# Kernel tuning notes

Hardware: AMD Instinct MI355X
Metric: run time of the kernel (lower is better)

The kernel has to match this reference:

```python
import jax, jax.numpy as jnp
import numpy as np

GRID_H, GRID_W, NUM_FEATURES = 512, 512, 4
N_POINTS = 8388608


def setup_inputs() -> dict:
    key = jax.random.key(0)
    k1, k2 = jax.random.split(key)
    feature_grid = jax.random.normal(k1, (GRID_H, GRID_W, NUM_FEATURES), dtype=jnp.float32)
    # continuous sample locations in grid coordinates [0, dim-1)
    u = jax.random.uniform(k2, (N_POINTS, 2), dtype=jnp.float32)
    location = u * jnp.array([GRID_H - 1, GRID_W - 1], dtype=jnp.float32)
    return {"feature_grid": feature_grid, "location": location}


def bilinear_sample(feature_grid, location):
    H, W, F = feature_grid.shape
    x = location[:, 0]
    y = location[:, 1]
    x0 = jnp.clip(jnp.floor(x), 0, H - 2).astype(jnp.int32)
    y0 = jnp.clip(jnp.floor(y), 0, W - 2).astype(jnp.int32)
    x1 = x0 + 1
    y1 = y0 + 1
    fx = (x - x0.astype(x.dtype))[:, None]  # [N,1]
    fy = (y - y0.astype(y.dtype))[:, None]
    # gather 4 corners: each [N,F]
    f00 = feature_grid[x0, y0]
    f01 = feature_grid[x0, y1]
    f10 = feature_grid[x1, y0]
    f11 = feature_grid[x1, y1]
    return (f00 * (1 - fx) * (1 - fy)
            + f01 * (1 - fx) * fy
            + f10 * fx * (1 - fy)
            + f11 * fx * fy)


def reference(feature_grid, location):
    return bilinear_sample(feature_grid, location)
```

## Files before the change

kernel.cpp:

```cpp
#include <hip/hip_runtime.h>
#include <hip/hip_fp16.h>

#define GRID_H 512
#define GRID_W 512
#define NCELLS (GRID_H * GRID_W)

typedef float f32x4 __attribute__((ext_vector_type(4)));

__global__ __launch_bounds__(256) void convert_grid_kernel(
    const float4* __restrict__ g,
    uint2* __restrict__ gh,
    int ncells)
{
    int i = blockIdx.x * blockDim.x + threadIdx.x;
    if (i < ncells) {
        float4 v = g[i];
        __half2 lo = __floats2half2_rn(v.x, v.y);
        __half2 hi = __floats2half2_rn(v.z, v.w);
        uint2 o;
        o.x = *reinterpret_cast<const unsigned int*>(&lo);
        o.y = *reinterpret_cast<const unsigned int*>(&hi);
        gh[i] = o;
    }
}

struct alignas(8) RowPair { __half2 h[4]; };

__device__ __forceinline__ f32x4 sample_point(const char* __restrict__ gh, float x, float y)
{
    float fx0 = fminf(fmaxf(floorf(x), 0.0f), (float)(GRID_H - 2));
    float fy0 = fminf(fmaxf(floorf(y), 0.0f), (float)(GRID_W - 2));
    int x0 = (int)fx0;
    int y0 = (int)fy0;
    float fx = x - fx0;
    float fy = y - fy0;

    int c0 = x0 * GRID_W + y0;

    RowPair r0 = *reinterpret_cast<const RowPair*>(gh + (size_t)c0 * 8);
    RowPair r1 = *reinterpret_cast<const RowPair*>(gh + (size_t)(c0 + GRID_W) * 8);

    float2 a0 = __half22float2(r0.h[0]);
    float2 a1 = __half22float2(r0.h[1]);
    float2 b0 = __half22float2(r0.h[2]);
    float2 b1 = __half22float2(r0.h[3]);
    float2 c0f = __half22float2(r1.h[0]);
    float2 c1f = __half22float2(r1.h[1]);
    float2 d0 = __half22float2(r1.h[2]);
    float2 d1 = __half22float2(r1.h[3]);

    float gx = 1.0f - fx;
    float gy = 1.0f - fy;
    float w00 = gx * gy;
    float w01 = gx * fy;
    float w10 = fx * gy;
    float w11 = fx * fy;

    f32x4 r;
    r.x = a0.x * w00 + b0.x * w01 + c0f.x * w10 + d0.x * w11;
    r.y = a0.y * w00 + b0.y * w01 + c0f.y * w10 + d0.y * w11;
    r.z = a1.x * w00 + b1.x * w01 + c1f.x * w10 + d1.x * w11;
    r.w = a1.y * w00 + b1.y * w01 + c1f.y * w10 + d1.y * w11;
    return r;
}

__global__ __launch_bounds__(256) void bilinear_half_kernel(
    const char* __restrict__ gh,
    const f32x4* __restrict__ loc2,
    f32x4* __restrict__ out,
    int npair, int n)
{
    const int stride = gridDim.x * blockDim.x;
    for (int i = blockIdx.x * blockDim.x + threadIdx.x; i < npair; i += stride) {
        f32x4 p = __builtin_nontemporal_load(&loc2[i]);
        f32x4 rA = sample_point(gh, p.x, p.y);
        f32x4 rB = sample_point(gh, p.z, p.w);
        __builtin_nontemporal_store(rA, &out[2 * i]);
        __builtin_nontemporal_store(rB, &out[2 * i + 1]);
    }
    if ((n & 1) && blockIdx.x == 0 && threadIdx.x == 0) {
        const float2* locs = (const float2*)loc2;
        float2 p = locs[n - 1];
        f32x4 r = sample_point(gh, p.x, p.y);
        out[n - 1] = r;
    }
}

__global__ __launch_bounds__(256) void bilinear_f32_kernel(
    const float4* __restrict__ grid,
    const float2* __restrict__ loc,
    float4* __restrict__ out,
    int n)
{
    const int stride = gridDim.x * blockDim.x;
    for (int i = blockIdx.x * blockDim.x + threadIdx.x; i < n; i += stride) {
        float2 p = loc[i];
        float fx0 = fminf(fmaxf(floorf(p.x), 0.0f), (float)(GRID_H - 2));
        float fy0 = fminf(fmaxf(floorf(p.y), 0.0f), (float)(GRID_W - 2));
        int x0 = (int)fx0, y0 = (int)fy0;
        float fx = p.x - fx0, fy = p.y - fy0;
        int base = x0 * GRID_W + y0;
        float4 f00 = grid[base];
        float4 f01 = grid[base + 1];
        float4 f10 = grid[base + GRID_W];
        float4 f11 = grid[base + GRID_W + 1];
        float gx = 1.0f - fx, gy = 1.0f - fy;
        float w00 = gx * gy, w01 = gx * fy, w10 = fx * gy, w11 = fx * fy;
        float4 r;
        r.x = f00.x * w00 + f01.x * w01 + f10.x * w10 + f11.x * w11;
        r.y = f00.y * w00 + f01.y * w01 + f10.y * w10 + f11.y * w11;
        r.z = f00.z * w00 + f01.z * w01 + f10.z * w10 + f11.z * w11;
        r.w = f00.w * w00 + f01.w * w01 + f10.w * w10 + f11.w * w11;
        out[i] = r;
    }
}

extern "C" void kernel_launch(void* const* d_in, const int* in_sizes, int n_in,
                              void* d_out, int out_size, void* d_ws, size_t ws_size,
                              hipStream_t stream) {
    const float* grid_f32 = (const float*)d_in[0];
    const float* loc_f32  = (const float*)d_in[1];

    int n = in_sizes[1] / 2;
    const size_t gh_bytes = (size_t)NCELLS * 8;

    if (ws_size >= gh_bytes) {
        {
            int threads = 256;
            int blocks = (NCELLS + threads - 1) / threads;
            convert_grid_kernel<<<blocks, threads, 0, stream>>>(
                (const float4*)grid_f32, (uint2*)d_ws, NCELLS);
        }
        {
            int npair = n / 2;
            const int block = 256;
            int blocks = (npair + block - 1) / block;
            if (blocks > 8192) blocks = 8192;
            if (blocks < 1) blocks = 1;
            bilinear_half_kernel<<<blocks, block, 0, stream>>>(
                (const char*)d_ws, (const f32x4*)loc_f32, (f32x4*)d_out, npair, n);
        }
    } else {
        const int block = 256;
        int blocks = (n + block - 1) / block;
        if (blocks > 8192) blocks = 8192;
        bilinear_f32_kernel<<<blocks, block, 0, stream>>>(
            (const float4*)grid_f32, (const float2*)loc_f32, (float4*)d_out, n);
    }
}
```

Baseline: 114.1 us.

## Pre-pack fp16 2x2 corner quads per cell for single contiguous gather

Adds a preprocessing kernel that, for each cell, packs the four fp16 corner feature vectors into one contiguous 32-byte record. Each sample then reads a single 32-byte region instead of two 16-byte loads from two separate grid rows, so fewer cache lines are touched per lookup. In exchange the packed grid is four times larger than the plain fp16 grid, which makes it less likely to stay resident in L2 under random access, and the build kernel adds extra writes. The fp32 fallback path for a small workspace is removed, and the row-pair fallback now assumes 16-byte alignment on addresses that are only 8-byte aligned.

```diff
diff --git a/kernel.cpp b/kernel.cpp
--- a/kernel.cpp
+++ b/kernel.cpp
@@ -7,10 +7,99 @@
 
 typedef float f32x4 __attribute__((ext_vector_type(4)));
 
+struct alignas(16) Half8 { __half2 h[4]; };
+
+__global__ __launch_bounds__(256) void build_quad_kernel(
+    const float4* __restrict__ g,
+    char* __restrict__ q)
+{
+    int i = blockIdx.x * blockDim.x + threadIdx.x;
+    if (i >= NCELLS) return;
+    int x = i >> 9;
+    int y = i & (GRID_W - 1);
+    if (x > GRID_H - 2) x = GRID_H - 2;
+    if (y > GRID_W - 2) y = GRID_W - 2;
+
+    float4 c00 = g[x * GRID_W + y];
+    float4 c01 = g[x * GRID_W + y + 1];
+    float4 c10 = g[(x + 1) * GRID_W + y];
+    float4 c11 = g[(x + 1) * GRID_W + y + 1];
+
+    Half8 q0, q1;
+    q0.h[0] = __floats2half2_rn(c00.x, c00.y);
+    q0.h[1] = __floats2half2_rn(c00.z, c00.w);
+    q0.h[2] = __floats2half2_rn(c01.x, c01.y);
+    q0.h[3] = __floats2half2_rn(c01.z, c01.w);
+    q1.h[0] = __floats2half2_rn(c10.x, c10.y);
+    q1.h[1] = __floats2half2_rn(c10.z, c10.w);
+    q1.h[2] = __floats2half2_rn(c11.x, c11.y);
+    q1.h[3] = __floats2half2_rn(c11.z, c11.w);
+
+    *reinterpret_cast<Half8*>(q + (size_t)i * 32)      = q0;
+    *reinterpret_cast<Half8*>(q + (size_t)i * 32 + 16) = q1;
+}
+
+__device__ __forceinline__ f32x4 sample_quad(const char* __restrict__ q, float x, float y)
+{
+    float fx0 = fminf(fmaxf(floorf(x), 0.0f), (float)(GRID_H - 2));
+    float fy0 = fminf(fmaxf(floorf(y), 0.0f), (float)(GRID_W - 2));
+    int x0 = (int)fx0;
+    int y0 = (int)fy0;
+    float fx = x - fx0;
+    float fy = y - fy0;
+
+    size_t off = ((size_t)(x0 << 9 | y0)) * 32;
+    Half8 r0 = *reinterpret_cast<const Half8*>(q + off);
+    Half8 r1 = *reinterpret_cast<const Half8*>(q + off + 16);
+
+    float2 a0 = __half22float2(r0.h[0]);
+    float2 a1 = __half22float2(r0.h[1]);
+    float2 b0 = __half22float2(r0.h[2]);
+    float2 b1 = __half22float2(r0.h[3]);
+    float2 c0 = __half22float2(r1.h[0]);
+    float2 c1 = __half22float2(r1.h[1]);
+    float2 d0 = __half22float2(r1.h[2]);
+    float2 d1 = __half22float2(r1.h[3]);
+
+    float gx = 1.0f - fx;
+    float gy = 1.0f - fy;
+    float w00 = gx * gy;
+    float w01 = gx * fy;
+    float w10 = fx * gy;
+    float w11 = fx * fy;
+
+    f32x4 r;
+    r.x = a0.x * w00 + b0.x * w01 + c0.x * w10 + d0.x * w11;
+    r.y = a0.y * w00 + b0.y * w01 + c0.y * w10 + d0.y * w11;
+    r.z = a1.x * w00 + b1.x * w01 + c1.x * w10 + d1.x * w11;
+    r.w = a1.y * w00 + b1.y * w01 + c1.y * w10 + d1.y * w11;
+    return r;
+}
+
+__global__ __launch_bounds__(256) void bilinear_quad_kernel(
+    const char* __restrict__ q,
+    const f32x4* __restrict__ loc2,
+    f32x4* __restrict__ out,
+    int npair, int n)
+{
+    const int stride = gridDim.x * blockDim.x;
+    for (int i = blockIdx.x * blockDim.x + threadIdx.x; i < npair; i += stride) {
+        f32x4 p = __builtin_nontemporal_load(&loc2[i]);
+        f32x4 rA = sample_quad(q, p.x, p.y);
+        f32x4 rB = sample_quad(q, p.z, p.w);
+        __builtin_nontemporal_store(rA, &out[2 * i]);
+        __builtin_nontemporal_store(rB, &out[2 * i + 1]);
+    }
+    if ((n & 1) && blockIdx.x == 0 && threadIdx.x == 0) {
+        const float2* locs = (const float2*)loc2;
+        float2 p = locs[n - 1];
+        f32x4 r = sample_quad(q, p.x, p.y);
+        out[n - 1] = r;
+    }
+}
+
 __global__ __launch_bounds__(256) void convert_grid_kernel(
-    const float4* __restrict__ g,
-    uint2* __restrict__ gh,
-    int ncells)
+    const float4* __restrict__ g, uint2* __restrict__ gh, int ncells)
 {
     int i = blockIdx.x * blockDim.x + threadIdx.x;
     if (i < ncells) {
@@ -24,22 +113,15 @@
     }
 }
 
-struct alignas(8) RowPair { __half2 h[4]; };
-
-__device__ __forceinline__ f32x4 sample_point(const char* __restrict__ gh, float x, float y)
+__device__ __forceinline__ f32x4 sample_rowpair(const char* __restrict__ gh, float x, float y)
 {
     float fx0 = fminf(fmaxf(floorf(x), 0.0f), (float)(GRID_H - 2));
     float fy0 = fminf(fmaxf(floorf(y), 0.0f), (float)(GRID_W - 2));
-    int x0 = (int)fx0;
-    int y0 = (int)fy0;
-    float fx = x - fx0;
-    float fy = y - fy0;
-
+    int x0 = (int)fx0, y0 = (int)fy0;
+    float fx = x - fx0, fy = y - fy0;
     int c0 = x0 * GRID_W + y0;
-
-    RowPair r0 = *reinterpret_cast<const RowPair*>(gh + (size_t)c0 * 8);
-    RowPair r1 = *reinterpret_cast<const RowPair*>(gh + (size_t)(c0 + GRID_W) * 8);
-
+    Half8 r0 = *reinterpret_cast<const Half8*>(gh + (size_t)c0 * 8);
+    Half8 r1 = *reinterpret_cast<const Half8*>(gh + (size_t)(c0 + GRID_W) * 8);
     float2 a0 = __half22float2(r0.h[0]);
     float2 a1 = __half22float2(r0.h[1]);
     float2 b0 = __half22float2(r0.h[2]);
@@ -48,14 +130,8 @@
     float2 c1f = __half22float2(r1.h[1]);
     float2 d0 = __half22float2(r1.h[2]);
     float2 d1 = __half22float2(r1.h[3]);
-
-    float gx = 1.0f - fx;
-    float gy = 1.0f - fy;
-    float w00 = gx * gy;
-    float w01 = gx * fy;
-    float w10 = fx * gy;
-    float w11 = fx * fy;
-
+    float gx = 1.0f - fx, gy = 1.0f - fy;
+    float w00 = gx * gy, w01 = gx * fy, w10 = fx * gy, w11 = fx * fy;
     f32x4 r;
     r.x = a0.x * w00 + b0.x * w01 + c0f.x * w10 + d0.x * w11;
     r.y = a0.y * w00 + b0.y * w01 + c0f.y * w10 + d0.y * w11;
@@ -65,53 +141,22 @@
 }
 
 __global__ __launch_bounds__(256) void bilinear_half_kernel(
-    const char* __restrict__ gh,
-    const f32x4* __restrict__ loc2,
-    f32x4* __restrict__ out,
-    int npair, int n)
+    const char* __restrict__ gh, const f32x4* __restrict__ loc2,
+    f32x4* __restrict__ out, int npair, int n)
 {
     const int stride = gridDim.x * blockDim.x;
     for (int i = blockIdx.x * blockDim.x + threadIdx.x; i < npair; i += stride) {
         f32x4 p = __builtin_nontemporal_load(&loc2[i]);
-        f32x4 rA = sample_point(gh, p.x, p.y);
-        f32x4 rB = sample_point(gh, p.z, p.w);
+        f32x4 rA = sample_rowpair(gh, p.x, p.y);
+        f32x4 rB = sample_rowpair(gh, p.z, p.w);
         __builtin_nontemporal_store(rA, &out[2 * i]);
         __builtin_nontemporal_store(rB, &out[2 * i + 1]);
     }
     if ((n & 1) && blockIdx.x == 0 && threadIdx.x == 0) {
         const float2* locs = (const float2*)loc2;
         float2 p = locs[n - 1];
-        f32x4 r = sample_point(gh, p.x, p.y);
+        f32x4 r = sample_rowpair(gh, p.x, p.y);
         out[n - 1] = r;
-    }
-}
-
-__global__ __launch_bounds__(256) void bilinear_f32_kernel(
-    const float4* __restrict__ grid,
-    const float2* __restrict__ loc,
-    float4* __restrict__ out,
-    int n)
-{
-    const int stride = gridDim.x * blockDim.x;
-    for (int i = blockIdx.x * blockDim.x + threadIdx.x; i < n; i += stride) {
-        float2 p = loc[i];
-        float fx0 = fminf(fmaxf(floorf(p.x), 0.0f), (float)(GRID_H - 2));
-        float fy0 = fminf(fmaxf(floorf(p.y), 0.0f), (float)(GRID_W - 2));
-        int x0 = (int)fx0, y0 = (int)fy0;
-        float fx = p.x - fx0, fy = p.y - fy0;
-        int base = x0 * GRID_W + y0;
-        float4 f00 = grid[base];
-        float4 f01 = grid[base + 1];
-        float4 f10 = grid[base + GRID_W];
-        float4 f11 = grid[base + GRID_W + 1];
-        float gx = 1.0f - fx, gy = 1.0f - fy;
-        float w00 = gx * gy, w01 = gx * fy, w10 = fx * gy, w11 = fx * fy;
-        float4 r;
-        r.x = f00.x * w00 + f01.x * w01 + f10.x * w10 + f11.x * w11;
-        r.y = f00.y * w00 + f01.y * w01 + f10.y * w10 + f11.y * w11;
-        r.z = f00.z * w00 + f01.z * w01 + f10.z * w10 + f11.z * w11;
-        r.w = f00.w * w00 + f01.w * w01 + f10.w * w10 + f11.w * w11;
-        out[i] = r;
     }
 }
 
@@ -122,29 +167,24 @@
     const float* loc_f32  = (const float*)d_in[1];
 
     int n = in_sizes[1] / 2;
-    const size_t gh_bytes = (size_t)NCELLS * 8;
+    int npair = n / 2;
+    const size_t quad_bytes = (size_t)NCELLS * 32;
+    const size_t gh_bytes   = (size_t)NCELLS * 8;
 
-    if (ws_size >= gh_bytes) {
-        {
-            int threads = 256;
-            int blocks = (NCELLS + threads - 1) / threads;
-            convert_grid_kernel<<<blocks, threads, 0, stream>>>(
-                (const float4*)grid_f32, (uint2*)d_ws, NCELLS);
-        }
-        {
-            int npair = n / 2;
-            const int block = 256;
-            int blocks = (npair + block - 1) / block;
-            if (blocks > 8192) blocks = 8192;
-            if (blocks < 1) blocks = 1;
-            bilinear_half_kernel<<<blocks, block, 0, stream>>>(
-                (const char*)d_ws, (const f32x4*)loc_f32, (f32x4*)d_out, npair, n);
-        }
-    } else {
-        const int block = 256;
-        int blocks = (n + block - 1) / block;
-        if (blocks > 8192) blocks = 8192;
-        bilinear_f32_kernel<<<blocks, block, 0, stream>>>(
-            (const float4*)grid_f32, (const float2*)loc_f32, (float4*)d_out, n);
+    const int block = 256;
+    int blocks = (npair + block - 1) / block;
+    if (blocks > 8192) blocks = 8192;
+    if (blocks < 1) blocks = 1;
+
+    if (ws_size >= quad_bytes) {
+        build_quad_kernel<<<(NCELLS + 255) / 256, 256, 0, stream>>>(
+            (const float4*)grid_f32, (char*)d_ws);
+        bilinear_quad_kernel<<<blocks, block, 0, stream>>>(
+            (const char*)d_ws, (const f32x4*)loc_f32, (f32x4*)d_out, npair, n);
+    } else if (ws_size >= gh_bytes) {
+        convert_grid_kernel<<<(NCELLS + 255) / 256, 256, 0, stream>>>(
+            (const float4*)grid_f32, (uint2*)d_ws, NCELLS);
+        bilinear_half_kernel<<<blocks, block, 0, stream>>>(
+            (const char*)d_ws, (const f32x4*)loc_f32, (f32x4*)d_out, npair, n);
     }
 }
```

Measured after the change: 122.8 us. +7.6%, slower.

## Replace fp16 grid with int8 per-cell corner quads using global absmax scale

Applied to the files above, without the earlier changes.

Precomputes, for every cell, the four bilinear corners of all four features quantized to int8 with a global absmax scale, packed into 16 bytes. The sampling kernel then does a single 16-byte gather per point instead of two row loads, folding the scale into the interpolation weights. It adds an absmax reduction pass with atomics, a quad-build pass and extra launches, and reduces precision to roughly 8 bits, which may exceed tolerance.

```diff
diff --git a/kernel.cpp b/kernel.cpp
--- a/kernel.cpp
+++ b/kernel.cpp
@@ -1,32 +1,81 @@
 #include <hip/hip_runtime.h>
-#include <hip/hip_fp16.h>
 
 #define GRID_H 512
 #define GRID_W 512
 #define NCELLS (GRID_H * GRID_W)
 
 typedef float f32x4 __attribute__((ext_vector_type(4)));
+typedef int   i32x4 __attribute__((ext_vector_type(4)));
 
-__global__ __launch_bounds__(256) void convert_grid_kernel(
-    const float4* __restrict__ g,
-    uint2* __restrict__ gh,
-    int ncells)
+#define WS_QUAD_OFF 256
+
+__global__ __launch_bounds__(64) void zero_scale_kernel(unsigned* s) {
+    if (threadIdx.x == 0) *s = 0u;
+}
+
+__global__ __launch_bounds__(256) void absmax_kernel(
+    const f32x4* __restrict__ g,
+    unsigned* __restrict__ out)
 {
     int i = blockIdx.x * blockDim.x + threadIdx.x;
-    if (i < ncells) {
-        float4 v = g[i];
-        __half2 lo = __floats2half2_rn(v.x, v.y);
-        __half2 hi = __floats2half2_rn(v.z, v.w);
-        uint2 o;
-        o.x = *reinterpret_cast<const unsigned int*>(&lo);
-        o.y = *reinterpret_cast<const unsigned int*>(&hi);
-        gh[i] = o;
-    }
+    f32x4 v = g[i];
+    float m = fmaxf(fmaxf(fabsf(v.x), fabsf(v.y)), fmaxf(fabsf(v.z), fabsf(v.w)));
+    #pragma unroll
+    for (int off = 32; off > 0; off >>= 1)
+        m = fmaxf(m, __shfl_down(m, off, 64));
+    if ((threadIdx.x & 63) == 0)
+        atomicMax(out, __float_as_uint(m));
 }
 
-struct alignas(8) RowPair { __half2 h[4]; };
+__device__ __forceinline__ int pack4(float a, float b, float c, float d, float inv)
+{
+    int qa = (int)rintf(fminf(fmaxf(a * inv, -127.f), 127.f));
+    int qb = (int)rintf(fminf(fmaxf(b * inv, -127.f), 127.f));
+    int qc = (int)rintf(fminf(fmaxf(c * inv, -127.f), 127.f));
+    int qd = (int)rintf(fminf(fmaxf(d * inv, -127.f), 127.f));
+    return (qa & 0xff) | ((qb & 0xff) << 8) | ((qc & 0xff) << 16) | ((qd & 0xff) << 24);
+}
 
-__device__ __forceinline__ f32x4 sample_point(const char* __restrict__ gh, float x, float y)
+__global__ __launch_bounds__(256) void build_quad_kernel(
+    const float4* __restrict__ g,
+    const unsigned* __restrict__ scale_bits,
+    i32x4* __restrict__ q)
+{
+    int i = blockIdx.x * blockDim.x + threadIdx.x;
+    if (i >= NCELLS) return;
+    int x = i >> 9;
+    int y = i & (GRID_W - 1);
+    if (x > GRID_H - 2) x = GRID_H - 2;
+    if (y > GRID_W - 2) y = GRID_W - 2;
+
+    float mx = __uint_as_float(*scale_bits);
+    float S = mx * (1.0f / 127.0f);
+    float inv = 1.0f / S;
+
+    float4 c00 = g[x * GRID_W + y];
+    float4 c01 = g[x * GRID_W + y + 1];
+    float4 c10 = g[(x + 1) * GRID_W + y];
+    float4 c11 = g[(x + 1) * GRID_W + y + 1];
+
+    i32x4 o;
+    o.x = pack4(c00.x, c01.x, c10.x, c11.x, inv);
+    o.y = pack4(c00.y, c01.y, c10.y, c11.y, inv);
+    o.z = pack4(c00.z, c01.z, c10.z, c11.z, inv);
+    o.w = pack4(c00.w, c01.w, c10.w, c11.w, inv);
+    q[i] = o;
+}
+
+__device__ __forceinline__ float dot_i8(int d, float w00, float w01, float w10, float w11)
+{
+    float f0 = (float)((d << 24) >> 24);
+    float f1 = (float)((d << 16) >> 24);
+    float f2 = (float)((d << 8) >> 24);
+    float f3 = (float)(d >> 24);
+    return f0 * w00 + f1 * w01 + f2 * w10 + f3 * w11;
+}
+
+__device__ __forceinline__ f32x4 sample_one(const i32x4* __restrict__ q, float S,
+                                            float x, float y)
 {
     float fx0 = fminf(fmaxf(floorf(x), 0.0f), (float)(GRID_H - 2));
     float fy0 = fminf(fmaxf(floorf(y), 0.0f), (float)(GRID_W - 2));
@@ -35,53 +84,43 @@
     float fx = x - fx0;
     float fy = y - fy0;
 
-    int c0 = x0 * GRID_W + y0;
-
-    RowPair r0 = *reinterpret_cast<const RowPair*>(gh + (size_t)c0 * 8);
-    RowPair r1 = *reinterpret_cast<const RowPair*>(gh + (size_t)(c0 + GRID_W) * 8);
-
-    float2 a0 = __half22float2(r0.h[0]);
-    float2 a1 = __half22float2(r0.h[1]);
-    float2 b0 = __half22float2(r0.h[2]);
-    float2 b1 = __half22float2(r0.h[3]);
-    float2 c0f = __half22float2(r1.h[0]);
-    float2 c1f = __half22float2(r1.h[1]);
-    float2 d0 = __half22float2(r1.h[2]);
-    float2 d1 = __half22float2(r1.h[3]);
+    i32x4 d = q[(x0 << 9) | y0];
 
     float gx = 1.0f - fx;
     float gy = 1.0f - fy;
-    float w00 = gx * gy;
-    float w01 = gx * fy;
-    float w10 = fx * gy;
-    float w11 = fx * fy;
+    float w00 = gx * gy * S;
+    float w01 = gx * fy * S;
+    float w10 = fx * gy * S;
+    float w11 = fx * fy * S;
 
     f32x4 r;
-    r.x = a0.x * w00 + b0.x * w01 + c0f.x * w10 + d0.x * w11;
-    r.y = a0.y * w00 + b0.y * w01 + c0f.y * w10 + d0.y * w11;
-    r.z = a1.x * w00 + b1.x * w01 + c1f.x * w10 + d1.x * w11;
-    r.w = a1.y * w00 + b1.y * w01 + c1f.y * w10 + d1.y * w11;
+    r.x = dot_i8(d.x, w00, w01, w10, w11);
+    r.y = dot_i8(d.y, w00, w01, w10, w11);
+    r.z = dot_i8(d.z, w00, w01, w10, w11);
+    r.w = dot_i8(d.w, w00, w01, w10, w11);
     return r;
 }
 
-__global__ __launch_bounds__(256) void bilinear_half_kernel(
-    const char* __restrict__ gh,
+__global__ __launch_bounds__(256) void sample_quad_i8_kernel(
+    const i32x4* __restrict__ q,
+    const unsigned* __restrict__ scale_bits,
     const f32x4* __restrict__ loc2,
     f32x4* __restrict__ out,
     int npair, int n)
 {
+    const float S = __uint_as_float(*scale_bits) * (1.0f / 127.0f);
     const int stride = gridDim.x * blockDim.x;
     for (int i = blockIdx.x * blockDim.x + threadIdx.x; i < npair; i += stride) {
         f32x4 p = __builtin_nontemporal_load(&loc2[i]);
-        f32x4 rA = sample_point(gh, p.x, p.y);
-        f32x4 rB = sample_point(gh, p.z, p.w);
+        f32x4 rA = sample_one(q, S, p.x, p.y);
+        f32x4 rB = sample_one(q, S, p.z, p.w);
         __builtin_nontemporal_store(rA, &out[2 * i]);
         __builtin_nontemporal_store(rB, &out[2 * i + 1]);
     }
     if ((n & 1) && blockIdx.x == 0 && threadIdx.x == 0) {
         const float2* locs = (const float2*)loc2;
         float2 p = locs[n - 1];
-        f32x4 r = sample_point(gh, p.x, p.y);
+        f32x4 r = sample_one(q, S, p.x, p.y);
         out[n - 1] = r;
     }
 }
@@ -122,29 +161,29 @@
     const float* loc_f32  = (const float*)d_in[1];
 
     int n = in_sizes[1] / 2;
-    const size_t gh_bytes = (size_t)NCELLS * 8;
+    int npair = n / 2;
+    const size_t need = WS_QUAD_OFF + (size_t)NCELLS * 16;
 
-    if (ws_size >= gh_bytes) {
-        {
-            int threads = 256;
-            int blocks = (NCELLS + threads - 1) / threads;
-            convert_grid_kernel<<<blocks, threads, 0, stream>>>(
-                (const float4*)grid_f32, (uint2*)d_ws, NCELLS);
-        }
-        {
-            int npair = n / 2;
-            const int block = 256;
-            int blocks = (npair + block - 1) / block;
-            if (blocks > 8192) blocks = 8192;
-            if (blocks < 1) blocks = 1;
-            bilinear_half_kernel<<<blocks, block, 0, stream>>>(
-                (const char*)d_ws, (const f32x4*)loc_f32, (f32x4*)d_out, npair, n);
-        }
+    const int block = 256;
+    int blocks = (npair + block - 1) / block;
+    if (blocks > 8192) blocks = 8192;
+    if (blocks < 1) blocks = 1;
+
+    if (ws_size >= need) {
+        unsigned* scale_bits = (unsigned*)d_ws;
+        i32x4* quads = (i32x4*)((char*)d_ws + WS_QUAD_OFF);
+
+        zero_scale_kernel<<<1, 64, 0, stream>>>(scale_bits);
+        absmax_kernel<<<NCELLS / 256, 256, 0, stream>>>(
+            (const f32x4*)grid_f32, scale_bits);
+        build_quad_kernel<<<(NCELLS + 255) / 256, 256, 0, stream>>>(
+            (const float4*)grid_f32, scale_bits, quads);
+        sample_quad_i8_kernel<<<blocks, block, 0, stream>>>(
+            quads, scale_bits, (const f32x4*)loc_f32, (f32x4*)d_out, npair, n);
     } else {
-        const int block = 256;
-        int blocks = (n + block - 1) / block;
-        if (blocks > 8192) blocks = 8192;
-        bilinear_f32_kernel<<<blocks, block, 0, stream>>>(
+        int blocks2 = (n + block - 1) / block;
+        if (blocks2 > 8192) blocks2 = 8192;
+        bilinear_f32_kernel<<<blocks2, block, 0, stream>>>(
             (const float4*)grid_f32, (const float2*)loc_f32, (float4*)d_out, n);
     }
 }
```

New measurement: 147.6 us. +29.3%, slower.
